# Performance work log

Hardware: AMD Instinct MI355X
Metric: run time of the kernel (lower is better)

## Reference

```python
import jax, jax.numpy as jnp
import numpy as np

N_STATE, N_CTRL, T, NB = 32, 16, 128, 64
NSC = N_STATE + N_CTRL

mT = lambda m: jnp.swapaxes(m, -1, -2)


def setup_inputs() -> dict:
    key = jax.random.key(0)
    k1, k2, k3, k4, k5, k6 = jax.random.split(key, 6)
    # Q must be PSD (the torch example builds Q = Qr^T Qr); add I for conditioning.
    Qr = jax.random.normal(k1, (NB, T, NSC, NSC), jnp.float32)
    Q = mT(Qr) @ Qr / NSC + jnp.eye(NSC, dtype=jnp.float32)
    p = jax.random.normal(k2, (NB, T, NSC), jnp.float32)
    x_init = jax.random.normal(k3, (NB, N_STATE), jnp.float32)
    # Stable-ish linear dynamics so the T=128 rollout does not blow up.
    A = jnp.tile(0.95 * jnp.eye(N_STATE, dtype=jnp.float32), (NB, 1, 1)) \
        + 0.02 * jax.random.normal(k4, (NB, N_STATE, N_STATE), jnp.float32)
    Bm = 0.1 * jax.random.normal(k5, (NB, N_STATE, N_CTRL), jnp.float32)
    c1 = 0.1 * jax.random.normal(k6, (NB, N_STATE), jnp.float32)
    return {"x_init": x_init, "Q": Q, "p": p, "A": A, "Bm": Bm, "c1": c1}


def _gains(Qt, qt, ns):
    # Qt: [B, nsc, nsc], qt: [B, nsc, 1]
    Qxx, Qxu = Qt[:, :ns, :ns], Qt[:, :ns, ns:]
    Qux, Quu = Qt[:, ns:, :ns], Qt[:, ns:, ns:]
    qx, qu = qt[:, :ns], qt[:, ns:]
    Quu_inv = jnp.linalg.pinv(Quu)          # batched pinv, as in the torch code
    K = -(Quu_inv @ Qux)                    # [B, nc, ns]
    k = -(Quu_inv @ qu)                     # [B, nc, 1]
    KT = mT(K)
    V = Qxx + Qxu @ K + KT @ Qux + KT @ Quu @ K
    v = qx + Qxu @ k + KT @ qu + KT @ Quu @ k
    return K, k, V, v


def _lqr(x_init, Q, p, A, Bm, c1):
    ns = A.shape[-1]
    F = jnp.concatenate([A, Bm], axis=-1)   # [B, ns, nsc]
    FT = mT(F)
    ft = c1[..., None]                       # [B, ns, 1]

    # ---- backward Riccati/DP recursion (sequential over T) ----
    K_last, k_last, V, v = _gains(Q[:, -1], p[:, -1][..., None], ns)

    def bstep(carry, inp):
        Vtp1, vtp1 = carry
        Qt_raw, pt = inp                     # [B,nsc,nsc], [B,nsc]
        Qt = Qt_raw + FT @ Vtp1 @ F
        qt = pt[..., None] + FT @ (Vtp1 @ ft) + FT @ vtp1
        K, k, Vt, vt = _gains(Qt, qt, ns)
        return (Vt, vt), (K, k)

    Qtm = jnp.swapaxes(Q[:, :-1], 0, 1)[::-1]   # [T-1, B, nsc, nsc], t = T-2..0
    ptm = jnp.swapaxes(p[:, :-1], 0, 1)[::-1]
    _, (Ks_rev, ks_rev) = jax.lax.scan(bstep, (V, v), (Qtm, ptm))
    Ks = jnp.concatenate([Ks_rev[::-1], K_last[None]], axis=0)  # [T, B, nc, ns], forward time order
    ks = jnp.concatenate([ks_rev[::-1], k_last[None]], axis=0)  # [T, B, nc, 1]

    # ---- forward rollout ----
    def fstep(x, inp):
        K, k, Qt, pt = inp
        u = jnp.einsum('bij,bj->bi', K, x) + k[..., 0]
        xu = jnp.concatenate([x, u], axis=-1)                 # tau_t, [B, nsc]
        obj = 0.5 * jnp.einsum('bi,bij,bj->b', xu, Qt, xu) + jnp.einsum('bi,bi->b', xu, pt)
        xn = jnp.einsum('bij,bj->bi', A, x) + jnp.einsum('bij,bj->bi', Bm, u) + c1
        return xn, (x, u, obj, xu)

    Qf = jnp.swapaxes(Q, 0, 1)               # [T, B, nsc, nsc]
    pf = jnp.swapaxes(p, 0, 1)
    _, (xs, us, objs, taus) = jax.lax.scan(fstep, x_init, (Ks, ks, Qf, pf))
    # xs: [T, B, ns] (x_0..x_{T-1}, matching torch which does not append x_T)
    return xs, us, objs, taus


def reference(x_init, Q, p, A, Bm, c1):
    return _lqr(x_init, Q, p, A, Bm, c1)
```

## Files before the change

kernel.cpp:

```cpp
#include <hip/hip_runtime.h>

#define TT     128
#define NBATCH 64

#define BAR()  asm volatile("s_waitcnt lgkmcnt(0)\n\ts_barrier" ::: "memory")
#define BARV() asm volatile("s_waitcnt vmcnt(0) lgkmcnt(0)\n\ts_barrier" ::: "memory")

__device__ __forceinline__ void gload16(const float* g, float* l) {
    __builtin_amdgcn_global_load_lds(
        (__attribute__((address_space(1))) void*)g,
        (__attribute__((address_space(3))) void*)l, 16, 0, 0);
}

__device__ __forceinline__ void inv4(const float4 pr[4], float IP[4][4]) {
    float a00=pr[0].x, a01=pr[0].y, a10=pr[1].x, a11=pr[1].y;
    float b00=pr[0].z, b01=pr[0].w, b10=pr[1].z, b11=pr[1].w;
    float c00=pr[2].x, c01=pr[2].y, c10=pr[3].x, c11=pr[3].y;
    float d00=pr[2].z, d01=pr[2].w, d10=pr[3].z, d11=pr[3].w;
    float r = 1.0f / (a00*a11 - a01*a10);
    float ia00 =  a11*r, ia01 = -a01*r, ia10 = -a10*r, ia11 = a00*r;
    float t00 = ia00*b00 + ia01*b10, t01 = ia00*b01 + ia01*b11;
    float t10 = ia10*b00 + ia11*b10, t11 = ia10*b01 + ia11*b11;
    float u00 = c00*ia00 + c01*ia10, u01 = c00*ia01 + c01*ia11;
    float u10 = c10*ia00 + c11*ia10, u11 = c10*ia01 + c11*ia11;
    float s00 = d00 - (c00*t00 + c01*t10), s01 = d01 - (c00*t01 + c01*t11);
    float s10 = d10 - (c10*t00 + c11*t10), s11 = d11 - (c10*t01 + c11*t11);
    float rs = 1.0f / (s00*s11 - s01*s10);
    float is00 =  s11*rs, is01 = -s01*rs, is10 = -s10*rs, is11 = s00*rs;
    float su00 = is00*u00 + is01*u10, su01 = is00*u01 + is01*u11;
    float su10 = is10*u00 + is11*u10, su11 = is10*u01 + is11*u11;
    IP[0][0] = ia00 + (t00*su00 + t01*su10);
    IP[0][1] = ia01 + (t00*su01 + t01*su11);
    IP[1][0] = ia10 + (t10*su00 + t11*su10);
    IP[1][1] = ia11 + (t10*su01 + t11*su11);
    IP[0][2] = -(t00*is00 + t01*is10);  IP[0][3] = -(t00*is01 + t01*is11);
    IP[1][2] = -(t10*is00 + t11*is10);  IP[1][3] = -(t10*is01 + t11*is11);
    IP[2][0] = -su00; IP[2][1] = -su01;
    IP[3][0] = -su10; IP[3][1] = -su11;
    IP[2][2] = is00;  IP[2][3] = is01;
    IP[3][2] = is10;  IP[3][3] = is11;
}

__global__ __launch_bounds__(256, 1)
void lqr_backward(const float* __restrict__ Q, const float* __restrict__ p,
                  const float* __restrict__ A, const float* __restrict__ Bm,
                  const float* __restrict__ c1, float* __restrict__ Kws)
{
    const int b   = blockIdx.x;
    const int tid = threadIdx.x;

    __shared__ __align__(16) float Fs[32*52];
    __shared__ __align__(16) float Vs[32*36];
    __shared__ __align__(16) float Ms[32*52];
    __shared__ __align__(16) float Xs[48*52];
    __shared__ __align__(16) float Qtb[2][48*48];
    __shared__ __align__(16) float qtb[2][256];
    __shared__ __align__(16) float Wa[16*52];
    __shared__ __align__(16) float Wb[16*52];
    __shared__ float vsv[32], fts[32], wv[32];

    for (int s = tid; s < 256; s += 256) {
        int k = s >> 3, q = s & 7;
        ((float4*)(Fs + k*52))[q] = ((const float4*)A)[(b*32 + k)*8 + q];
    }
    for (int s = tid; s < 128; s += 256) {
        int k = s >> 2, q = s & 3;
        ((float4*)(Fs + k*52))[8 + q] = ((const float4*)Bm)[(b*32 + k)*4 + q];
    }
    for (int s = tid; s < 288; s += 256) ((float4*)Vs)[s] = make_float4(0,0,0,0);
    if (tid < 32) { vsv[tid] = 0.0f; fts[tid] = c1[b*32 + tid]; }

    {
        const float* Qs0 = Q + (size_t)(b*TT + TT-1) * 2304;
        #pragma unroll
        for (int r = 0; r < 3; ++r) {
            int e = r*256 + tid;
            if (e < 576) gload16(Qs0 + e*4, Qtb[0] + e*4);
        }
        if (tid < 12) gload16(p + (size_t)(b*TT + TT-1)*48 + tid*4, qtb[0] + tid*4);
    }
    BARV();

    for (int t = TT-1; t >= 0; --t) {
        const int cur = (TT-1 - t) & 1;
        float* Qtc = Qtb[cur];
        float* qtc = qtb[cur];

        if (tid < 96) {
            const int i0 = (tid/12)*4, c0 = (tid%12)*4;
            float4 a0 = make_float4(0,0,0,0), a1 = a0, a2 = a0, a3 = a0;
            #pragma unroll
            for (int k = 0; k < 32; ++k) {
                float4 v = *(const float4*)(Vs + k*36 + i0);
                float4 f = *(const float4*)(Fs + k*52 + c0);
                a0.x += v.x*f.x; a0.y += v.x*f.y; a0.z += v.x*f.z; a0.w += v.x*f.w;
                a1.x += v.y*f.x; a1.y += v.y*f.y; a1.z += v.y*f.z; a1.w += v.y*f.w;
                a2.x += v.z*f.x; a2.y += v.z*f.y; a2.z += v.z*f.z; a2.w += v.z*f.w;
                a3.x += v.w*f.x; a3.y += v.w*f.y; a3.z += v.w*f.z; a3.w += v.w*f.w;
            }
            *(float4*)(Ms + (i0+0)*52 + c0) = a0;
            *(float4*)(Ms + (i0+1)*52 + c0) = a1;
            *(float4*)(Ms + (i0+2)*52 + c0) = a2;
            *(float4*)(Ms + (i0+3)*52 + c0) = a3;
        } else if (tid >= 192) {
            const int idx = tid - 192;
            if (t > 0) {
                const float* Qs = Q + (size_t)(b*TT + t-1) * 2304;
                float* dst = Qtb[cur ^ 1];
                #pragma unroll
                for (int r = 0; r < 9; ++r) {
                    int e = r*64 + idx;
                    gload16(Qs + e*4, dst + e*4);
                }
                if (idx < 12) gload16(p + (size_t)(b*TT + t-1)*48 + idx*4,
                                      qtb[cur ^ 1] + idx*4);
            }
            if (idx < 32) {
                float acc = vsv[idx];
                #pragma unroll
                for (int k = 0; k < 32; ++k) acc += Vs[idx*36 + k] * fts[k];
                wv[idx] = acc;
            }
        }
        BAR();

        if (tid < 144) {
            const int r0 = (tid/12)*4, c0 = (tid%12)*4;
            float4 a0 = *(const float4*)(Qtc + (r0+0)*48 + c0);
            float4 a1 = *(const float4*)(Qtc + (r0+1)*48 + c0);
            float4 a2 = *(const float4*)(Qtc + (r0+2)*48 + c0);
            float4 a3 = *(const float4*)(Qtc + (r0+3)*48 + c0);
            #pragma unroll
            for (int k = 0; k < 32; ++k) {
                float4 fr = *(const float4*)(Fs + k*52 + r0);
                float4 mc = *(const float4*)(Ms + k*52 + c0);
                a0.x += fr.x*mc.x; a0.y += fr.x*mc.y; a0.z += fr.x*mc.z; a0.w += fr.x*mc.w;
                a1.x += fr.y*mc.x; a1.y += fr.y*mc.y; a1.z += fr.y*mc.z; a1.w += fr.y*mc.w;
                a2.x += fr.z*mc.x; a2.y += fr.z*mc.y; a2.z += fr.z*mc.z; a2.w += fr.z*mc.w;
                a3.x += fr.w*mc.x; a3.y += fr.w*mc.y; a3.z += fr.w*mc.z; a3.w += fr.w*mc.w;
            }
            *(float4*)(Xs + (r0+0)*52 + c0) = a0;
            *(float4*)(Xs + (r0+1)*52 + c0) = a1;
            *(float4*)(Xs + (r0+2)*52 + c0) = a2;
            *(float4*)(Xs + (r0+3)*52 + c0) = a3;
        } else if (tid >= 192 && tid < 240) {
            const int c = tid - 192;
            float acc = qtc[c];
            #pragma unroll
            for (int k = 0; k < 32; ++k) acc += Fs[k*52 + c] * wv[k];
            qtc[c] = acc;
            if (c >= 32) Xs[c*52 + 48] = acc;
        }
        BAR();

        float* Kbase = Kws + (size_t)(b*TT + t) * 528;
        #pragma unroll
        for (int q = 0; q < 4; ++q) {
            const float* S = (q == 0) ? (Xs + 32*52) : ((q & 1) ? Wa : Wb);
            float*       D = (q & 1) ? Wb : Wa;
            const int pc = 4*q;

            float4 pr[4];
            #pragma unroll
            for (int m = 0; m < 4; ++m)
                pr[m] = *(const float4*)(S + (4*q + m)*52 + 32 + pc);
            float IP[4][4];
            inv4(pr, IP);

            if (tid < 196) {
                const int c  = tid >> 2;
                const int rg = tid & 3;
                float sn[4], R[4];
                #pragma unroll
                for (int n = 0; n < 4; ++n) sn[n] = S[(4*q + n)*52 + c];
                #pragma unroll
                for (int m = 0; m < 4; ++m)
                    R[m] = IP[m][0]*sn[0] + IP[m][1]*sn[1] + IP[m][2]*sn[2] + IP[m][3]*sn[3];

                #pragma unroll
                for (int i2 = 0; i2 < 4; ++i2) {
                    const int r = 4*rg + i2;
                    float val;
                    if (rg == q) {
                        val = R[i2];
                    } else {
                        float4 f = *(const float4*)(S + r*52 + 32 + pc);
                        float src = S[r*52 + c];
                        val = src - (f.x*R[0] + f.y*R[1] + f.z*R[2] + f.w*R[3]);
                    }
                    D[r*52 + c] = val;
                    if (q == 3) {
                        if (c < 32)       Kbase[c*16 + r] = -val;
                        else if (c == 48) Kbase[512 + r]  = -val;
                    }
                }
            }
            BAR();
        }

        {
            const int i = tid >> 3, j0 = (tid & 7) * 4;
            float4 acc = *(const float4*)(Xs + i*52 + j0);
            float qxu[16];
            #pragma unroll
            for (int m = 0; m < 4; ++m) {
                float4 v4 = *(const float4*)(Xs + i*52 + 32 + m*4);
                qxu[m*4+0] = v4.x; qxu[m*4+1] = v4.y;
                qxu[m*4+2] = v4.z; qxu[m*4+3] = v4.w;
            }
            #pragma unroll
            for (int k = 0; k < 16; ++k) {
                float4 kk = *(const float4*)(Wb + k*52 + j0);
                acc.x -= qxu[k]*kk.x; acc.y -= qxu[k]*kk.y;
                acc.z -= qxu[k]*kk.z; acc.w -= qxu[k]*kk.w;
            }
            *(float4*)(Vs + i*36 + j0) = acc;
            if ((tid & 7) == 0) {
                float accv = qtc[i];
                #pragma unroll
                for (int k = 0; k < 16; ++k)
                    accv -= qxu[k] * Wb[k*52 + 48];
                vsv[i] = accv;
            }
        }
        BARV();
    }
}

__global__ __launch_bounds__(64, 1)
void lqr_forward(const float* __restrict__ Kws, const float* __restrict__ A,
                 const float* __restrict__ Bm, const float* __restrict__ c1,
                 const float* __restrict__ x_init,
                 float* __restrict__ xs, float* __restrict__ us,
                 float* __restrict__ taus)
{
    const int b = blockIdx.x, l = threadIdx.x;
    __shared__ __align__(16) float Fb[32*48];
    __shared__ __align__(16) float Kb[544];
    __shared__ float c1s[32], xu[48];

    for (int s = l; s < 256; s += 64) {
        int k = s >> 3, q = s & 7;
        ((float4*)Fb)[k*12 + q] = ((const float4*)A)[(b*32 + k)*8 + q];
    }
    for (int s = l; s < 128; s += 64) {
        int k = s >> 2, q = s & 3;
        ((float4*)Fb)[k*12 + 8 + q] = ((const float4*)Bm)[(b*32 + k)*4 + q];
    }
    if (l < 32) { c1s[l] = c1[b*32 + l]; xu[l] = x_init[b*32 + l]; }

    float4 ka, kb, kc = make_float4(0,0,0,0);
    {
        const float4* s0 = (const float4*)(Kws + (size_t)(b*TT) * 528);
        ka = s0[l]; kb = s0[l + 64];
        if (l < 4) kc = s0[l + 128];
    }
    __syncthreads();

    for (int t = 0; t < TT; ++t) {
        ((float4*)Kb)[l]      = ka;
        ((float4*)Kb)[l + 64] = kb;
        if (l < 4) ((float4*)Kb)[l + 128] = kc;
        __syncthreads();

        if (t + 1 < TT) {
            const float4* sn = (const float4*)(Kws + (size_t)(b*TT + t+1) * 528);
            ka = sn[l]; kb = sn[l + 64];
            if (l < 4) kc = sn[l + 128];
        }

        float part = 0.0f;
        int i = l & 15, g = l >> 4;
        #pragma unroll
        for (int jj = 0; jj < 8; ++jj) {
            int j = g*8 + jj;
            part += Kb[j*16 + i] * xu[j];
        }
        part += __shfl_down(part, 32);
        part += __shfl_down(part, 16);
        float ui = part + Kb[512 + i];
        if (l < 16) {
            xu[32 + l] = ui;
            us[(size_t)(t*64 + b)*16 + l] = ui;
        }
        __syncthreads();

        if (l < 32) xs[(size_t)(t*64 + b)*32 + l] = xu[l];
        if (l < 48) taus[(size_t)(t*64 + b)*48 + l] = xu[l];

        float pn = 0.0f;
        int i2 = l & 31, h = l >> 5;
        #pragma unroll
        for (int jj = 0; jj < 24; ++jj) {
            int j = h*24 + jj;
            pn += Fb[i2*48 + j] * xu[j];
        }
        pn += __shfl_down(pn, 32);
        float xni = pn + ((l < 32) ? c1s[i2] : 0.0f);
        __syncthreads();
        if (l < 32) xu[l] = xni;
        __syncthreads();
    }
}

__global__ __launch_bounds__(256, 4)
void lqr_obj(const float* __restrict__ Q, const float* __restrict__ p,
             const float* __restrict__ taus, float* __restrict__ objs)
{
    const int bi = blockIdx.x;
    const int b = bi >> 7, t = bi & 127;
    const int tid = threadIdx.x;
    __shared__ float xu[48];
    __shared__ float red[8];
    const float* tp = taus + (size_t)(t*64 + b)*48;
    if (tid < 48) xu[tid] = tp[tid];
    __syncthreads();

    const float4* Q4 = (const float4*)(Q + (size_t)bi * 2304);
    float acc = 0.0f;
    for (int e4 = tid; e4 < 576; e4 += 256) {
        float4 qv = Q4[e4];
        int r = e4 / 12, c = (e4 % 12) * 4;
        float xr = xu[r];
        acc += xr * (qv.x*xu[c] + qv.y*xu[c+1] + qv.z*xu[c+2] + qv.w*xu[c+3]);
    }
    acc *= 0.5f;
    if (tid < 48) acc += xu[tid] * p[(size_t)bi*48 + tid];

    #pragma unroll
    for (int off = 32; off > 0; off >>= 1) acc += __shfl_down(acc, off);
    if ((tid & 63) == 0) red[tid >> 6] = acc;
    __syncthreads();
    if (tid == 0) objs[(t << 6) + b] = red[0] + red[1] + red[2] + red[3];
}

extern "C" void kernel_launch(void* const* d_in, const int* in_sizes, int n_in,
                              void* d_out, int out_size, void* d_ws, size_t ws_size,
                              hipStream_t stream) {
    const float* x_init = (const float*)d_in[0];
    const float* Q      = (const float*)d_in[1];
    const float* p      = (const float*)d_in[2];
    const float* A      = (const float*)d_in[3];
    const float* Bm     = (const float*)d_in[4];
    const float* c1     = (const float*)d_in[5];

    float* out  = (float*)d_out;
    float* xs   = out;
    float* us   = out + 262144;
    float* objs = out + 393216;
    float* taus = out + 401408;

    float* Kws = (float*)d_ws;

    lqr_backward<<<NBATCH, 256, 0, stream>>>(Q, p, A, Bm, c1, Kws);
    lqr_forward<<<NBATCH, 64, 0, stream>>>(Kws, A, Bm, c1, x_init, xs, us, taus);
    lqr_obj<<<NBATCH*TT, 256, 0, stream>>>(Q, p, taus, objs);
}
```

Baseline: 780.6 us.

## Keep F column slice in registers and retile V·F and F^T·M products

Each thread now loads a fixed 4-column slice of F=[A|B] for all 32 rows into 32 float4 registers once at kernel start. The V·F product is split across 192 threads computing 2 rows each instead of 96 threads computing 4 rows. The F^T·M product is remapped so each thread's output rows come from its register slice, leaving only one LDS read per k. The aim is fewer LDS loads and more parallelism in the per-step serial chain, at the cost of 128 extra VGPRs per thread, which raises register pressure and the chance of spills. The unroll pragma on the 4-block inversion loop is also removed.

Result: slower. 990.1 us (+26.8%).

```diff
diff --git a/kernel.cpp b/kernel.cpp
--- a/kernel.cpp
+++ b/kernel.cpp
@@ -48,6 +48,7 @@
 {
     const int b   = blockIdx.x;
     const int tid = threadIdx.x;
+    const int s   = tid % 12;
 
     __shared__ __align__(16) float Fs[32*52];
     __shared__ __align__(16) float Vs[32*36];
@@ -59,15 +60,22 @@
     __shared__ __align__(16) float Wb[16*52];
     __shared__ float vsv[32], fts[32], wv[32];
 
-    for (int s = tid; s < 256; s += 256) {
-        int k = s >> 3, q = s & 7;
+    float4 fsl[32];
+    #pragma unroll
+    for (int k = 0; k < 32; ++k) {
+        if (s < 8) fsl[k] = *(const float4*)(A  + (size_t)(b*32 + k)*32 + 4*s);
+        else       fsl[k] = *(const float4*)(Bm + (size_t)(b*32 + k)*16 + 4*(s-8));
+    }
+
+    for (int st = tid; st < 256; st += 256) {
+        int k = st >> 3, q = st & 7;
         ((float4*)(Fs + k*52))[q] = ((const float4*)A)[(b*32 + k)*8 + q];
     }
-    for (int s = tid; s < 128; s += 256) {
-        int k = s >> 2, q = s & 3;
+    for (int st = tid; st < 128; st += 256) {
+        int k = st >> 2, q = st & 3;
         ((float4*)(Fs + k*52))[8 + q] = ((const float4*)Bm)[(b*32 + k)*4 + q];
     }
-    for (int s = tid; s < 288; s += 256) ((float4*)Vs)[s] = make_float4(0,0,0,0);
+    for (int st = tid; st < 288; st += 256) ((float4*)Vs)[st] = make_float4(0,0,0,0);
     if (tid < 32) { vsv[tid] = 0.0f; fts[tid] = c1[b*32 + tid]; }
 
     {
@@ -86,23 +94,19 @@
         float* Qtc = Qtb[cur];
         float* qtc = qtb[cur];
 
-        if (tid < 96) {
-            const int i0 = (tid/12)*4, c0 = (tid%12)*4;
-            float4 a0 = make_float4(0,0,0,0), a1 = a0, a2 = a0, a3 = a0;
+        if (tid < 192) {
+            const int r0 = 2 * (tid / 12);
+            float4 a0 = make_float4(0,0,0,0), a1 = a0;
             #pragma unroll
             for (int k = 0; k < 32; ++k) {
-                float4 v = *(const float4*)(Vs + k*36 + i0);
-                float4 f = *(const float4*)(Fs + k*52 + c0);
+                float2 v = *(const float2*)(Vs + k*36 + r0);
+                float4 f = fsl[k];
                 a0.x += v.x*f.x; a0.y += v.x*f.y; a0.z += v.x*f.z; a0.w += v.x*f.w;
                 a1.x += v.y*f.x; a1.y += v.y*f.y; a1.z += v.y*f.z; a1.w += v.y*f.w;
-                a2.x += v.z*f.x; a2.y += v.z*f.y; a2.z += v.z*f.z; a2.w += v.z*f.w;
-                a3.x += v.w*f.x; a3.y += v.w*f.y; a3.z += v.w*f.z; a3.w += v.w*f.w;
-            }
-            *(float4*)(Ms + (i0+0)*52 + c0) = a0;
-            *(float4*)(Ms + (i0+1)*52 + c0) = a1;
-            *(float4*)(Ms + (i0+2)*52 + c0) = a2;
-            *(float4*)(Ms + (i0+3)*52 + c0) = a3;
-        } else if (tid >= 192) {
+            }
+            *(float4*)(Ms + (r0  )*52 + 4*s) = a0;
+            *(float4*)(Ms + (r0+1)*52 + 4*s) = a1;
+        } else {
             const int idx = tid - 192;
             if (t > 0) {
                 const float* Qs = Q + (size_t)(b*TT + t-1) * 2304;
@@ -125,24 +129,25 @@
         BAR();
 
         if (tid < 144) {
-            const int r0 = (tid/12)*4, c0 = (tid%12)*4;
-            float4 a0 = *(const float4*)(Qtc + (r0+0)*48 + c0);
-            float4 a1 = *(const float4*)(Qtc + (r0+1)*48 + c0);
-            float4 a2 = *(const float4*)(Qtc + (r0+2)*48 + c0);
-            float4 a3 = *(const float4*)(Qtc + (r0+3)*48 + c0);
+            const int cq = tid / 12;
+            const int rb = 4 * s;
+            float4 a0 = *(const float4*)(Qtc + (rb+0)*48 + 4*cq);
+            float4 a1 = *(const float4*)(Qtc + (rb+1)*48 + 4*cq);
+            float4 a2 = *(const float4*)(Qtc + (rb+2)*48 + 4*cq);
+            float4 a3 = *(const float4*)(Qtc + (rb+3)*48 + 4*cq);
             #pragma unroll
             for (int k = 0; k < 32; ++k) {
-                float4 fr = *(const float4*)(Fs + k*52 + r0);
-                float4 mc = *(const float4*)(Ms + k*52 + c0);
-                a0.x += fr.x*mc.x; a0.y += fr.x*mc.y; a0.z += fr.x*mc.z; a0.w += fr.x*mc.w;
-                a1.x += fr.y*mc.x; a1.y += fr.y*mc.y; a1.z += fr.y*mc.z; a1.w += fr.y*mc.w;
-                a2.x += fr.z*mc.x; a2.y += fr.z*mc.y; a2.z += fr.z*mc.z; a2.w += fr.z*mc.w;
-                a3.x += fr.w*mc.x; a3.y += fr.w*mc.y; a3.z += fr.w*mc.z; a3.w += fr.w*mc.w;
-            }
-            *(float4*)(Xs + (r0+0)*52 + c0) = a0;
-            *(float4*)(Xs + (r0+1)*52 + c0) = a1;
-            *(float4*)(Xs + (r0+2)*52 + c0) = a2;
-            *(float4*)(Xs + (r0+3)*52 + c0) = a3;
+                float4 m4 = *(const float4*)(Ms + k*52 + 4*cq);
+                float4 f  = fsl[k];
+                a0.x += f.x*m4.x; a0.y += f.x*m4.y; a0.z += f.x*m4.z; a0.w += f.x*m4.w;
+                a1.x += f.y*m4.x; a1.y += f.y*m4.y; a1.z += f.y*m4.z; a1.w += f.y*m4.w;
+                a2.x += f.z*m4.x; a2.y += f.z*m4.y; a2.z += f.z*m4.z; a2.w += f.z*m4.w;
+                a3.x += f.w*m4.x; a3.y += f.w*m4.y; a3.z += f.w*m4.z; a3.w += f.w*m4.w;
+            }
+            *(float4*)(Xs + (rb+0)*52 + 4*cq) = a0;
+            *(float4*)(Xs + (rb+1)*52 + 4*cq) = a1;
+            *(float4*)(Xs + (rb+2)*52 + 4*cq) = a2;
+            *(float4*)(Xs + (rb+3)*52 + 4*cq) = a3;
         } else if (tid >= 192 && tid < 240) {
             const int c = tid - 192;
             float acc = qtc[c];
@@ -154,7 +159,6 @@
         BAR();
 
         float* Kbase = Kws + (size_t)(b*TT + t) * 528;
-        #pragma unroll
         for (int q = 0; q < 4; ++q) {
             const float* S = (q == 0) ? (Xs + 32*52) : ((q & 1) ? Wa : Wb);
             float*       D = (q & 1) ? Wb : Wa;
@@ -239,12 +243,12 @@
     __shared__ __align__(16) float Kb[544];
     __shared__ float c1s[32], xu[48];
 
-    for (int s = l; s < 256; s += 64) {
-        int k = s >> 3, q = s & 7;
+    for (int st = l; st < 256; st += 64) {
+        int k = st >> 3, q = st & 7;
         ((float4*)Fb)[k*12 + q] = ((const float4*)A)[(b*32 + k)*8 + q];
     }
-    for (int s = l; s < 128; s += 64) {
-        int k = s >> 2, q = s & 3;
+    for (int st = l; st < 128; st += 64) {
+        int k = st >> 2, q = st & 3;
         ((float4*)Fb)[k*12 + 8 + q] = ((const float4*)Bm)[(b*32 + k)*4 + q];
     }
     if (l < 32) { c1s[l] = c1[b*32 + l]; xu[l] = x_init[b*32 + l]; }
```
